# Optimization experiments

Measured on AMD Instinct MI355X. Metric: run time of the kernel, lower is better.

The kernel has to match this reference:

```python
import jax, jax.numpy as jnp
import numpy as np

B, C, N, M = 8, 128, 2048, 512

def setup_inputs() -> dict:
    key = jax.random.key(0)
    k1, k2, k3, k4 = jax.random.split(key, 4)
    scale = 1.0 / np.sqrt(C)
    x = jax.random.normal(k1, (B, C, N), dtype=jnp.float32)
    # conv1d with kernel size 1 and no bias == channel-mixing matmul, weight [C_out, C_in]
    Wq = jax.random.normal(k2, (C, C), dtype=jnp.float32) * scale
    Wk = jax.random.normal(k3, (C, C), dtype=jnp.float32) * scale
    Wv = jax.random.normal(k4, (C, C), dtype=jnp.float32) * scale
    return {"x": x, "Wq": Wq, "Wk": Wk, "Wv": Wv, "npts_ds": M}

def reference(x, Wq, Wk, Wv, npts_ds):
    # q,k,v: [B,C,N] via 1x1 conv == einsum over input channels
    q = jnp.einsum('oc,bcn->bon', Wq, x)
    k = jnp.einsum('oc,bcn->bon', Wk, x)
    v = jnp.einsum('oc,bcn->bon', Wv, x)
    # energy: [B,N,N] = q^T k (contract channel dim)
    energy = jnp.einsum('bcn,bcm->bnm', q, k)
    scale_factor = jnp.sqrt(jnp.asarray(q.shape[-2], dtype=energy.dtype))  # sqrt(C)
    attention = jax.nn.softmax(energy / scale_factor, axis=-1)  # [B,N,N]
    selection = jnp.sum(attention, axis=-2)  # [B,N] column sums
    _, idx = jax.lax.top_k(selection, npts_ds)  # [B,M]
    # gather selected attention rows: [B,M,N]
    scores = jnp.take_along_axis(attention, idx[:, :, None], axis=1)
    # weighted sum of values: [B,M,C]
    out = jnp.einsum('bmn,bcn->bcm', scores, v)  # [B,C,M]
    return out
```

## Files before the change

kernel.cpp:

```cpp
#include <hip/hip_runtime.h>
#include <math.h>

namespace {
constexpr int B = 8, C = 128, N = 2048, M = 512;
constexpr int NSPLIT = 8;
constexpr int MBLK = 16;
constexpr float INV_SQRT_C = 0.08838834764831845f;
}

typedef __attribute__((ext_vector_type(8))) short short8;
typedef __attribute__((ext_vector_type(16))) float f32x16;
typedef unsigned short ushort_t;
typedef unsigned int u32;

__device__ inline ushort_t f2bf(float f) {
  union { float f; u32 u; } a; a.f = f;
  u32 r = a.u + 0x7fffu + ((a.u >> 16) & 1u);
  return (ushort_t)(r >> 16);
}
__device__ inline float bf2f(ushort_t h) {
  union { u32 u; float f; } a; a.u = ((u32)h) << 16; return a.f;
}

__device__ __forceinline__ void gl_lds16(const ushort_t* g, ushort_t* l) {
  __builtin_amdgcn_global_load_lds(
      (const __attribute__((address_space(1))) unsigned int*)g,
      (__attribute__((address_space(3))) unsigned int*)l, 16, 0, 0);
}

__global__ __launch_bounds__(256) void qkv_kernel(
    const float* __restrict__ x, const float* __restrict__ Wq,
    const float* __restrict__ Wk, const float* __restrict__ Wv,
    ushort_t* __restrict__ split, ushort_t* __restrict__ vbf) {
  const size_t TERM = (size_t)B * N * C;
  int kc = blockIdx.x;
  int o0 = kc * 8;
  int n = blockIdx.y * 256 + threadIdx.x;
  int b = blockIdx.z;
  const float* xb = x + (size_t)b * C * N + n;
  float aq[8] = {}, ak[8] = {}, av[8] = {};
  #pragma unroll 4
  for (int c = 0; c < C; ++c) {
    float xv = xb[(size_t)c * N];
    #pragma unroll
    for (int j = 0; j < 8; ++j) {
      aq[j] = fmaf(Wq[(o0 + j) * C + c], xv, aq[j]);
      ak[j] = fmaf(Wk[(o0 + j) * C + c], xv, ak[j]);
      av[j] = fmaf(Wv[(o0 + j) * C + c], xv, av[j]);
    }
  }
  #pragma unroll
  for (int j = 0; j < 8; ++j)
    vbf[((size_t)b * C + o0 + j) * N + n] = f2bf(av[j]);
  size_t rowoff = ((size_t)b * 16 + kc) * (size_t)N * 8 + (size_t)n * 8;
  #pragma unroll
  for (int tt = 0; tt < 3; ++tt) {
    short8 qv, kv;
    #pragma unroll
    for (int j = 0; j < 8; ++j) {
      ushort_t h = f2bf(aq[j]); qv[j] = (short)h; aq[j] -= bf2f(h);
      h = f2bf(ak[j]);          kv[j] = (short)h; ak[j] -= bf2f(h);
    }
    *(short8*)&split[tt * TERM + rowoff]       = qv;
    *(short8*)&split[(3 + tt) * TERM + rowoff] = kv;
  }
}

__global__ __launch_bounds__(256) void energy_kernel(
    const ushort_t* __restrict__ split,
    float* __restrict__ Ae, float* __restrict__ rowpart) {
  __shared__ __align__(16) union {
    ushort_t stg[2][12288];
    struct { float red[128][64]; float red2[128][2]; } r;
  } sm;
  const size_t TERM = (size_t)B * N * C;
  const size_t ROW8 = (size_t)N * 8;
  int t = threadIdx.x;
  int lane = t & 63, w = t >> 6;
  int wn = w & 1, wm = w >> 1;
  int lin = blockIdx.y * 16 + blockIdx.x;
  int xcd = lin & 7, slot = lin >> 3;
  int st = xcd * 2 + (slot >> 4);
  int wi = slot & 15;
  int mb = (st & 3) * 4 + (wi & 3);
  int nb = (st >> 2) * 4 + (wi >> 2);
  int m0 = mb * 128, n0 = nb * 128, b = blockIdx.z;
  int lr = lane & 31, lq = lane >> 5;

  const ushort_t* gA = split + (size_t)b * 16 * ROW8
                     + (size_t)(t >> 7) * ROW8 + ((size_t)n0 + (t & 127)) * 8;
  const ushort_t* gB = split + 3 * TERM + (size_t)b * 16 * ROW8
                     + (size_t)(t >> 7) * ROW8 + ((size_t)m0 + (t & 127)) * 8;
  const int aoff = (lq * 128 + wn * 64 + lr) * 8;
  const int boff = (lq * 128 + wm * 64 + lr) * 8;

#define STAGE_STEP(buf_, s_) do {                                            \
    size_t so_ = (size_t)(2 * (s_)) * ROW8;                                  \
    _Pragma("unroll")                                                        \
    for (int tt = 0; tt < 3; ++tt) {                                         \
      gl_lds16(gA + (size_t)tt * TERM + so_, &sm.stg[buf_][tt * 2048 + t * 8]); \
      gl_lds16(gB + (size_t)tt * TERM + so_, &sm.stg[buf_][(3 + tt) * 2048 + t * 8]); \
    }                                                                        \
  } while (0)

  f32x16 acc[2][2] = {};
  STAGE_STEP(0, 0);
  STAGE_STEP(1, 1);
  #pragma unroll
  for (int s = 0; s < 8; ++s) {
    const int cur = s & 1;
    if (s < 7) asm volatile("s_waitcnt vmcnt(6)" ::: "memory");
    else       asm volatile("s_waitcnt vmcnt(0)" ::: "memory");
    __builtin_amdgcn_sched_barrier(0);
    __builtin_amdgcn_s_barrier();
    short8 aT[3][2], bT[3][2];
    #pragma unroll
    for (int tt = 0; tt < 3; ++tt)
      #pragma unroll
      for (int i = 0; i < 2; ++i) {
        aT[tt][i] = *(const short8*)&sm.stg[cur][tt * 2048 + aoff + i * 256];
        bT[tt][i] = *(const short8*)&sm.stg[cur][(3 + tt) * 2048 + boff + i * 256];
      }
    #pragma unroll
    for (int mt = 0; mt < 2; ++mt)
      #pragma unroll
      for (int nt = 0; nt < 2; ++nt) {
        acc[mt][nt] = __builtin_amdgcn_mfma_f32_32x32x16_bf16(aT[0][mt], bT[0][nt], acc[mt][nt], 0, 0, 0);
        acc[mt][nt] = __builtin_amdgcn_mfma_f32_32x32x16_bf16(aT[1][mt], bT[0][nt], acc[mt][nt], 0, 0, 0);
        acc[mt][nt] = __builtin_amdgcn_mfma_f32_32x32x16_bf16(aT[0][mt], bT[1][nt], acc[mt][nt], 0, 0, 0);
        acc[mt][nt] = __builtin_amdgcn_mfma_f32_32x32x16_bf16(aT[2][mt], bT[0][nt], acc[mt][nt], 0, 0, 0);
        acc[mt][nt] = __builtin_amdgcn_mfma_f32_32x32x16_bf16(aT[1][mt], bT[1][nt], acc[mt][nt], 0, 0, 0);
        acc[mt][nt] = __builtin_amdgcn_mfma_f32_32x32x16_bf16(aT[0][mt], bT[2][nt], acc[mt][nt], 0, 0, 0);
      }
    __builtin_amdgcn_sched_barrier(0);
    __builtin_amdgcn_s_barrier();
    if (s < 6) STAGE_STEP(cur, s + 2);
  }
#undef STAGE_STEP
  int lc = lr;
  #pragma unroll
  for (int mt = 0; mt < 2; ++mt) {
    #pragma unroll
    for (int reg = 0; reg < 16; ++reg) {
      int row = (reg & 3) + 8 * (reg >> 2) + 4 * lq;
      int rloc = wn * 64 + mt * 32 + row;
      float e0 = expf(acc[mt][0][reg] * INV_SQRT_C);
      float e1 = expf(acc[mt][1][reg] * INV_SQRT_C);
      float* pA = Ae + ((size_t)b * N + n0 + rloc) * N + m0 + wm * 64 + lc;
      __builtin_nontemporal_store(e0, pA);
      __builtin_nontemporal_store(e1, pA + 32);
      sm.r.red[rloc][wm * 32 + lc] = e0 + e1;
    }
  }
  __syncthreads();
  {
    int row = t >> 1, h = t & 1;
    float ssum = 0.f;
    #pragma unroll
    for (int j0 = 0; j0 < 32; ++j0) {
      int j = (j0 + (t & 31)) & 31;
      ssum += sm.r.red[row][h * 32 + j];
    }
    sm.r.red2[row][h] = ssum;
  }
  __syncthreads();
  if (t < 128)
    rowpart[(size_t)mb * (B * N) + b * N + n0 + t] = sm.r.red2[t][0] + sm.r.red2[t][1];
}

__global__ __launch_bounds__(256) void colsum_kernel(
    const float* __restrict__ Ae, const float* __restrict__ rowpart,
    float* __restrict__ selpart) {
  __shared__ float sinv[256];
  int t = threadIdx.x;
  int m = blockIdx.x * 256 + t;
  int nch = blockIdx.y, b = blockIdx.z;
  int n0 = nch * (N / 8);
  {
    int n = n0 + t;
    float s = 0.f;
    #pragma unroll
    for (int sl = 0; sl < MBLK; ++sl)
      s += rowpart[(size_t)sl * (B * N) + b * N + n];
    sinv[t] = 1.0f / s;
  }
  __syncthreads();
  const float* Ab = Ae + (size_t)b * N * N;
  float acc = 0.f;
  #pragma unroll 8
  for (int n = n0; n < n0 + N / 8; ++n)
    acc = fmaf(Ab[(size_t)n * N + m], sinv[n - n0], acc);
  selpart[(size_t)nch * (B * N) + b * N + m] = acc;
}

__global__ __launch_bounds__(256) void topk_kernel(
    const float* __restrict__ selpart, int* __restrict__ idx) {
  __shared__ float s[N];
  __shared__ int rsum[64][4];
  int b = blockIdx.y;
  int t = threadIdx.x;
  for (int i = t; i < N; i += 256) {
    float v_ = 0.f;
    #pragma unroll
    for (int nch = 0; nch < 8; ++nch)
      v_ += selpart[(size_t)nch * (B * N) + b * N + i];
    s[i] = v_;
  }
  __syncthreads();
  int i = blockIdx.x * 64 + (t & 63);
  int jc = t >> 6;
  float val = s[i];
  int r = 0;
  for (int j = jc * 512; j < jc * 512 + 512; ++j) {
    float sj = s[j];
    r += (sj > val || (sj == val && j < i)) ? 1 : 0;
  }
  rsum[t & 63][jc] = r;
  __syncthreads();
  if (t < 64) {
    int rank = rsum[t][0] + rsum[t][1] + rsum[t][2] + rsum[t][3];
    if (rank < M) idx[b * M + rank] = blockIdx.x * 64 + t;
  }
}

__global__ __launch_bounds__(256) void out_kernel(
    const float* __restrict__ Ae, const float* __restrict__ rowpart,
    const ushort_t* __restrict__ vbf, const int* __restrict__ idx,
    float* __restrict__ part) {
  __shared__ ushort_t sc[64][72];
  __shared__ ushort_t vt[128][72];
  __shared__ int ridx[64];
  __shared__ float rinv[64];
  int t = threadIdx.x;
  int m0 = blockIdx.x * 64;
  int ns = blockIdx.y;
  int b = blockIdx.z;
  if (t < 64) {
    int r = idx[b * M + m0 + t];
    ridx[t] = r;
    float s = 0.f;
    #pragma unroll
    for (int sl = 0; sl < MBLK; ++sl)
      s += rowpart[(size_t)sl * (B * N) + b * N + r];
    rinv[t] = 1.0f / s;
  }
  __syncthreads();
  int lane = t & 63, w = t >> 6;
  int wc = w & 1, wm = w >> 1;
  int lr = lane & 31, lq = lane >> 5;
  f32x16 acc[2] = {};
  int nbeg = ns * (N / NSPLIT);
  for (int kb = 0; kb < N / NSPLIT; kb += 64) {
    __syncthreads();
    #pragma unroll
    for (int it = 0; it < 16; ++it) {
      int ii = it * 256 + t;
      int r = ii >> 6, cn = ii & 63;
      float sv = Ae[((size_t)b * N + ridx[r]) * N + nbeg + kb + cn] * rinv[r];
      sc[r][cn] = f2bf(sv);
    }
    #pragma unroll
    for (int it = 0; it < 4; ++it) {
      int u = it * 256 + t;
      int r = u >> 3, seg = u & 7;
      *(short8*)&vt[r][seg * 8] =
          *(const short8*)&vbf[((size_t)b * C + r) * N + nbeg + kb + seg * 8];
    }
    __syncthreads();
    #pragma unroll
    for (int ks = 0; ks < 4; ++ks) {
      short8 bf_ = *(const short8*)&sc[wm * 32 + lr][ks * 16 + lq * 8];
      #pragma unroll
      for (int ct = 0; ct < 2; ++ct) {
        short8 af = *(const short8*)&vt[wc * 64 + ct * 32 + lr][ks * 16 + lq * 8];
        acc[ct] = __builtin_amdgcn_mfma_f32_32x32x16_bf16(af, bf_, acc[ct], 0, 0, 0);
      }
    }
  }
  float* pb = part + ((size_t)ns * B + b) * C * M;
  #pragma unroll
  for (int ct = 0; ct < 2; ++ct) {
    #pragma unroll
    for (int reg = 0; reg < 16; ++reg) {
      int crow = wc * 64 + ct * 32 + (reg & 3) + 8 * (reg >> 2) + 4 * lq;
      pb[(size_t)crow * M + m0 + wm * 32 + lr] = acc[ct][reg];
    }
  }
}

__global__ __launch_bounds__(256) void reduce_kernel(
    const float* __restrict__ part, float* __restrict__ out) {
  int i = (blockIdx.x * 256 + threadIdx.x) * 4;
  float4 a = make_float4(0.f, 0.f, 0.f, 0.f);
  #pragma unroll
  for (int ns = 0; ns < NSPLIT; ++ns) {
    float4 p = *(const float4*)&part[(size_t)ns * (B * C * M) + i];
    a.x += p.x; a.y += p.y; a.z += p.z; a.w += p.w;
  }
  *(float4*)&out[i] = a;
}

extern "C" void kernel_launch(void* const* d_in, const int* in_sizes, int n_in,
                              void* d_out, int out_size, void* d_ws, size_t ws_size,
                              hipStream_t stream) {
  const float* x  = (const float*)d_in[0];
  const float* Wq = (const float*)d_in[1];
  const float* Wk = (const float*)d_in[2];
  const float* Wv = (const float*)d_in[3];
  float* out = (float*)d_out;

  const size_t TSZ = (size_t)B * N * C;
  ushort_t* split = (ushort_t*)d_ws;
  ushort_t* vbf   = split + 6 * TSZ;
  float* Ae       = (float*)(vbf + TSZ);
  float* rowpart  = Ae + (size_t)B * N * N;
  float* selpart  = rowpart + (size_t)MBLK * B * N;
  int*   idx      = (int*)(selpart + (size_t)8 * B * N);
  float* part     = (float*)split;

  qkv_kernel<<<dim3(16, N / 256, B), 256, 0, stream>>>(x, Wq, Wk, Wv, split, vbf);
  energy_kernel<<<dim3(N / 128, N / 128, B), 256, 0, stream>>>(split, Ae, rowpart);
  colsum_kernel<<<dim3(N / 256, 8, B), 256, 0, stream>>>(Ae, rowpart, selpart);
  topk_kernel<<<dim3(N / 64, B), 256, 0, stream>>>(selpart, idx);
  out_kernel<<<dim3(M / 64, NSPLIT, B), 256, 0, stream>>>(Ae, rowpart, vbf, idx, part);
  reduce_kernel<<<dim3(B * C * M / 1024), 256, 0, stream>>>(part, out);
}
```

Baseline: 227.4 us.

## Widen energy kernel tile to 128x256 to reuse A operand across more columns

The energy GEMM tile grows from 128x128 to 128x256 along the key dimension. Each wave now holds 2x4 accumulators, the B operand staging buffer doubles, and the XCD-aware block remap changes to match the halved grid. Each CTA now writes two rowpart partial slices. The aim is to cut redundant global/LDS loads of the query split terms and amortize sync overhead. The cost is more accumulator registers, more LDS per block and fewer blocks in flight.

Result: slower. 234.3 us (+3.1%).

```diff
diff --git a/kernel.cpp b/kernel.cpp
--- a/kernel.cpp
+++ b/kernel.cpp
@@ -66,65 +66,69 @@
   }
 }
 
-__global__ __launch_bounds__(256) void energy_kernel(
+__global__ __launch_bounds__(256, 2) void energy_kernel(
     const ushort_t* __restrict__ split,
     float* __restrict__ Ae, float* __restrict__ rowpart) {
   __shared__ __align__(16) union {
-    ushort_t stg[2][12288];
-    struct { float red[128][64]; float red2[128][2]; } r;
+    ushort_t stg[2][18432];
+    struct { float red[2][128][64]; float red2[2][128][2]; } r;
   } sm;
   const size_t TERM = (size_t)B * N * C;
   const size_t ROW8 = (size_t)N * 8;
   int t = threadIdx.x;
   int lane = t & 63, w = t >> 6;
   int wn = w & 1, wm = w >> 1;
-  int lin = blockIdx.y * 16 + blockIdx.x;
-  int xcd = lin & 7, slot = lin >> 3;
-  int st = xcd * 2 + (slot >> 4);
-  int wi = slot & 15;
-  int mb = (st & 3) * 4 + (wi & 3);
-  int nb = (st >> 2) * 4 + (wi >> 2);
-  int m0 = mb * 128, n0 = nb * 128, b = blockIdx.z;
+  int lin = blockIdx.y * 8 + blockIdx.x;
+  int xcd = lin & 7, wi = lin >> 3;
+  int mbx = (xcd >> 1) * 2 + (wi & 1);
+  int nb  = (xcd & 1) * 8 + (wi >> 1);
+  int m0 = mbx * 256, n0 = nb * 128, b = blockIdx.z;
   int lr = lane & 31, lq = lane >> 5;
 
   const ushort_t* gA = split + (size_t)b * 16 * ROW8
                      + (size_t)(t >> 7) * ROW8 + ((size_t)n0 + (t & 127)) * 8;
-  const ushort_t* gB = split + 3 * TERM + (size_t)b * 16 * ROW8
-                     + (size_t)(t >> 7) * ROW8 + ((size_t)m0 + (t & 127)) * 8;
+  const ushort_t* gB0 = split + 3 * TERM + (size_t)b * 16 * ROW8
+                      + ((size_t)m0 + t) * 8;
+  const ushort_t* gB1 = gB0 + ROW8;
   const int aoff = (lq * 128 + wn * 64 + lr) * 8;
-  const int boff = (lq * 128 + wm * 64 + lr) * 8;
+  const int boffb = (lq * 256 + wm * 128 + lr) * 8;
 
 #define STAGE_STEP(buf_, s_) do {                                            \
     size_t so_ = (size_t)(2 * (s_)) * ROW8;                                  \
     _Pragma("unroll")                                                        \
     for (int tt = 0; tt < 3; ++tt) {                                         \
       gl_lds16(gA + (size_t)tt * TERM + so_, &sm.stg[buf_][tt * 2048 + t * 8]); \
-      gl_lds16(gB + (size_t)tt * TERM + so_, &sm.stg[buf_][(3 + tt) * 2048 + t * 8]); \
+      gl_lds16(gB0 + (size_t)tt * TERM + so_,                                \
+               &sm.stg[buf_][6144 + tt * 4096 + t * 8]);                     \
+      gl_lds16(gB1 + (size_t)tt * TERM + so_,                                \
+               &sm.stg[buf_][6144 + tt * 4096 + (t + 256) * 8]);             \
     }                                                                        \
   } while (0)
 
-  f32x16 acc[2][2] = {};
+  f32x16 acc[2][4] = {};
   STAGE_STEP(0, 0);
   STAGE_STEP(1, 1);
   #pragma unroll
   for (int s = 0; s < 8; ++s) {
     const int cur = s & 1;
-    if (s < 7) asm volatile("s_waitcnt vmcnt(6)" ::: "memory");
+    if (s < 7) asm volatile("s_waitcnt vmcnt(9)" ::: "memory");
     else       asm volatile("s_waitcnt vmcnt(0)" ::: "memory");
     __builtin_amdgcn_sched_barrier(0);
     __builtin_amdgcn_s_barrier();
-    short8 aT[3][2], bT[3][2];
-    #pragma unroll
-    for (int tt = 0; tt < 3; ++tt)
-      #pragma unroll
-      for (int i = 0; i < 2; ++i) {
+    short8 aT[3][2], bT[3][4];
+    #pragma unroll
+    for (int tt = 0; tt < 3; ++tt) {
+      #pragma unroll
+      for (int i = 0; i < 2; ++i)
         aT[tt][i] = *(const short8*)&sm.stg[cur][tt * 2048 + aoff + i * 256];
-        bT[tt][i] = *(const short8*)&sm.stg[cur][(3 + tt) * 2048 + boff + i * 256];
-      }
+      #pragma unroll
+      for (int nt = 0; nt < 4; ++nt)
+        bT[tt][nt] = *(const short8*)&sm.stg[cur][6144 + tt * 4096 + boffb + nt * 256];
+    }
     #pragma unroll
     for (int mt = 0; mt < 2; ++mt)
       #pragma unroll
-      for (int nt = 0; nt < 2; ++nt) {
+      for (int nt = 0; nt < 4; ++nt) {
         acc[mt][nt] = __builtin_amdgcn_mfma_f32_32x32x16_bf16(aT[0][mt], bT[0][nt], acc[mt][nt], 0, 0, 0);
         acc[mt][nt] = __builtin_amdgcn_mfma_f32_32x32x16_bf16(aT[1][mt], bT[0][nt], acc[mt][nt], 0, 0, 0);
         acc[mt][nt] = __builtin_amdgcn_mfma_f32_32x32x16_bf16(aT[0][mt], bT[1][nt], acc[mt][nt], 0, 0, 0);
@@ -144,28 +148,38 @@
     for (int reg = 0; reg < 16; ++reg) {
       int row = (reg & 3) + 8 * (reg >> 2) + 4 * lq;
       int rloc = wn * 64 + mt * 32 + row;
-      float e0 = expf(acc[mt][0][reg] * INV_SQRT_C);
-      float e1 = expf(acc[mt][1][reg] * INV_SQRT_C);
-      float* pA = Ae + ((size_t)b * N + n0 + rloc) * N + m0 + wm * 64 + lc;
-      __builtin_nontemporal_store(e0, pA);
-      __builtin_nontemporal_store(e1, pA + 32);
-      sm.r.red[rloc][wm * 32 + lc] = e0 + e1;
+      #pragma unroll
+      for (int h = 0; h < 2; ++h) {
+        float e0 = expf(acc[mt][2 * h][reg] * INV_SQRT_C);
+        float e1 = expf(acc[mt][2 * h + 1][reg] * INV_SQRT_C);
+        float* pA = Ae + ((size_t)b * N + n0 + rloc) * N + m0 + wm * 128 + h * 64 + lc;
+        __builtin_nontemporal_store(e0, pA);
+        __builtin_nontemporal_store(e1, pA + 32);
+        sm.r.red[wm][rloc][h * 32 + lc] = e0 + e1;
+      }
     }
   }
   __syncthreads();
   {
-    int row = t >> 1, h = t & 1;
-    float ssum = 0.f;
-    #pragma unroll
-    for (int j0 = 0; j0 < 32; ++j0) {
-      int j = (j0 + (t & 31)) & 31;
-      ssum += sm.r.red[row][h * 32 + j];
-    }
-    sm.r.red2[row][h] = ssum;
-  }
-  __syncthreads();
-  if (t < 128)
-    rowpart[(size_t)mb * (B * N) + b * N + n0 + t] = sm.r.red2[t][0] + sm.r.red2[t][1];
+    int row = t >> 1, h2 = t & 1;
+    #pragma unroll
+    for (int tile = 0; tile < 2; ++tile) {
+      float ssum = 0.f;
+      #pragma unroll
+      for (int j0 = 0; j0 < 32; ++j0) {
+        int j = (j0 + (t & 31)) & 31;
+        ssum += sm.r.red[tile][row][h2 * 32 + j];
+      }
+      sm.r.red2[tile][row][h2] = ssum;
+    }
+  }
+  __syncthreads();
+  if (t < 128) {
+    #pragma unroll
+    for (int tile = 0; tile < 2; ++tile)
+      rowpart[(size_t)(2 * mbx + tile) * (B * N) + b * N + n0 + t] =
+          sm.r.red2[tile][t][0] + sm.r.red2[tile][t][1];
+  }
 }
 
 __global__ __launch_bounds__(256) void colsum_kernel(
@@ -319,7 +333,7 @@
   float* part     = (float*)split;
 
   qkv_kernel<<<dim3(16, N / 256, B), 256, 0, stream>>>(x, Wq, Wk, Wv, split, vbf);
-  energy_kernel<<<dim3(N / 128, N / 128, B), 256, 0, stream>>>(split, Ae, rowpart);
+  energy_kernel<<<dim3(N / 256, N / 128, B), 256, 0, stream>>>(split, Ae, rowpart);
   colsum_kernel<<<dim3(N / 256, 8, B), 256, 0, stream>>>(Ae, rowpart, selpart);
   topk_kernel<<<dim3(N / 64, B), 256, 0, stream>>>(selpart, idx);
   out_kernel<<<dim3(M / 64, NSPLIT, B), 256, 0, stream>>>(Ae, rowpart, vbf, idx, part);
```

## Double-buffer colsum attention rows through LDS with async global-to-LDS loads

Applied to the files above, without the earlier changes.

Rewrites the column-sum kernel so it streams 32-row chunks of the normalized-energy matrix into a two-stage LDS buffer using global_load_lds, then accumulates from LDS. Each chunk load overlaps with the FMAs on the previous chunk, replacing the serial per-row strided global loads. It adds 64KB of LDS per block, which may cut occupancy, plus explicit waitcnt and barrier handling.

New measurement: 232.9 us. 1.02x slower.

```diff
diff --git a/kernel.cpp b/kernel.cpp
--- a/kernel.cpp
+++ b/kernel.cpp
@@ -23,6 +23,11 @@
 }
 
 __device__ __forceinline__ void gl_lds16(const ushort_t* g, ushort_t* l) {
+  __builtin_amdgcn_global_load_lds(
+      (const __attribute__((address_space(1))) unsigned int*)g,
+      (__attribute__((address_space(3))) unsigned int*)l, 16, 0, 0);
+}
+__device__ __forceinline__ void gl_lds16f(const float* g, float* l) {
   __builtin_amdgcn_global_load_lds(
       (const __attribute__((address_space(1))) unsigned int*)g,
       (__attribute__((address_space(3))) unsigned int*)l, 16, 0, 0);
@@ -171,26 +176,49 @@
 __global__ __launch_bounds__(256) void colsum_kernel(
     const float* __restrict__ Ae, const float* __restrict__ rowpart,
     float* __restrict__ selpart) {
+  __shared__ __align__(16) float stg[2][32 * 256];
   __shared__ float sinv[256];
   int t = threadIdx.x;
-  int m = blockIdx.x * 256 + t;
+  int lane = t & 63, w = t >> 6;
+  int m0 = blockIdx.x * 256;
   int nch = blockIdx.y, b = blockIdx.z;
   int n0 = nch * (N / 8);
   {
-    int n = n0 + t;
     float s = 0.f;
     #pragma unroll
     for (int sl = 0; sl < MBLK; ++sl)
-      s += rowpart[(size_t)sl * (B * N) + b * N + n];
+      s += rowpart[(size_t)sl * (B * N) + b * N + n0 + t];
     sinv[t] = 1.0f / s;
   }
   __syncthreads();
   const float* Ab = Ae + (size_t)b * N * N;
+#define CSTAGE(buf_, s_) do {                                                \
+    _Pragma("unroll")                                                        \
+    for (int j = 0; j < 8; ++j) {                                            \
+      int rl = j * 4 + w;                                                    \
+      gl_lds16f(Ab + (size_t)(n0 + (s_) * 32 + rl) * N + m0 + lane * 4,      \
+                &stg[buf_][rl * 256 + lane * 4]);                            \
+    }                                                                        \
+  } while (0)
   float acc = 0.f;
-  #pragma unroll 8
-  for (int n = n0; n < n0 + N / 8; ++n)
-    acc = fmaf(Ab[(size_t)n * N + m], sinv[n - n0], acc);
-  selpart[(size_t)nch * (B * N) + b * N + m] = acc;
+  CSTAGE(0, 0);
+  CSTAGE(1, 1);
+  #pragma unroll
+  for (int s = 0; s < 8; ++s) {
+    const int cur = s & 1;
+    if (s < 7) asm volatile("s_waitcnt vmcnt(8)" ::: "memory");
+    else       asm volatile("s_waitcnt vmcnt(0)" ::: "memory");
+    __builtin_amdgcn_sched_barrier(0);
+    __builtin_amdgcn_s_barrier();
+    #pragma unroll
+    for (int j = 0; j < 32; ++j)
+      acc = fmaf(stg[cur][j * 256 + t], sinv[s * 32 + j], acc);
+    __builtin_amdgcn_sched_barrier(0);
+    __builtin_amdgcn_s_barrier();
+    if (s < 6) CSTAGE(cur, s + 2);
+  }
+#undef CSTAGE
+  selpart[(size_t)nch * (B * N) + b * N + m0 + t] = acc;
 }
 
 __global__ __launch_bounds__(256) void topk_kernel(
```
